# Performance work log

Hardware: AMD Instinct MI355X
Metric: run time of the kernel (lower is better)

Reference implementation:

```python
import jax, jax.numpy as jnp
import numpy as np

D_MODEL = 512
N_HEADS = 8
HEAD_SIZE = 64


def setup_inputs() -> dict:
    key = jax.random.key(0)
    ks = jax.random.split(key, 6)
    B, T = 4, 2048
    x_q = jax.random.normal(ks[0], (B, T, D_MODEL), dtype=jnp.float32)
    s = 1.0 / np.sqrt(D_MODEL)
    # per-head q/k/v projection weights, stacked: [H, head_size, d_model]
    Wq = jax.random.normal(ks[1], (N_HEADS, HEAD_SIZE, D_MODEL), dtype=jnp.float32) * s
    Wk = jax.random.normal(ks[2], (N_HEADS, HEAD_SIZE, D_MODEL), dtype=jnp.float32) * s
    Wv = jax.random.normal(ks[3], (N_HEADS, HEAD_SIZE, D_MODEL), dtype=jnp.float32) * s
    Wp = jax.random.normal(ks[4], (D_MODEL, D_MODEL), dtype=jnp.float32) * s
    bp = jax.random.normal(ks[5], (D_MODEL,), dtype=jnp.float32) * 0.01
    return {"x_q": x_q, "Wq": Wq, "Wk": Wk, "Wv": Wv, "Wp": Wp, "bp": bp}


def reference(x_q, Wq, Wk, Wv, Wp, bp):
    B, T, C = x_q.shape  # C == d_model
    # per-head projections: [B, H, T, K]
    q = jnp.einsum('btd,hkd->bhtk', x_q, Wq)
    k = jnp.einsum('btd,hkd->bhtk', x_q, Wk)
    v = jnp.einsum('btd,hkd->bhtk', x_q, Wv)
    # NOTE: original scales by C**-0.5 with C = d_model (not head_size)
    scores = jnp.einsum('bhtk,bhsk->bhts', q, k) * (C ** -0.5)
    causal = jnp.tril(jnp.ones((T, T), dtype=bool))
    scores = jnp.where(causal, scores, -jnp.inf)
    wei = jax.nn.softmax(scores, axis=-1)  # dropout is identity in eval
    out = jnp.einsum('bhts,bhsk->bhtk', wei, v)
    # concat heads: [B, T, H*K] == [B, T, d_model]
    out = out.transpose(0, 2, 1, 3).reshape(B, T, C)
    return out @ Wp.T + bp
```

## Files before the change

kernel.cpp:

```cpp
#include <hip/hip_runtime.h>
#include <hip/hip_bf16.h>

using bf16x8 = __attribute__((ext_vector_type(8))) __bf16;
using f32x4  = __attribute__((ext_vector_type(4))) float;
using f32x16 = __attribute__((ext_vector_type(16))) float;
using i32x4  = __attribute__((ext_vector_type(4))) int;

#define MFMA_16x16x32(a, b, c) __builtin_amdgcn_mfma_f32_16x16x32_bf16((a), (b), (c), 0, 0, 0)
#define MFMA32(a, b, c)        __builtin_amdgcn_mfma_f32_32x32x16_bf16((a), (b), (c), 0, 0, 0)

#define GLOAD16(g, l)                                                         \
    __builtin_amdgcn_global_load_lds(                                         \
        (const __attribute__((address_space(1))) unsigned int*)(g),           \
        (__attribute__((address_space(3))) unsigned int*)(l), 16, 0, 0)

__device__ __forceinline__ ushort f2bf(float f) {
    return __builtin_bit_cast(ushort, (__bf16)f);
}
__device__ __forceinline__ float bf2f(ushort u) {
    union { unsigned int i; float f; } x; x.i = ((unsigned int)u) << 16; return x.f;
}
__device__ __forceinline__ unsigned pk_bf16(float lo, float hi) {
    unsigned r;
    asm volatile("v_cvt_pk_bf16_f32 %0, %1, %2" : "=v"(r) : "v"(lo), "v"(hi));
    return r;
}
__device__ __forceinline__ void pl32_swap(unsigned &a, unsigned &b) {
    asm volatile("v_permlane32_swap_b32 %0, %1" : "+v"(a), "+v"(b));
}

#define ENC(t, a, b) ((t) | ((a) << 8) | ((b) << 16))
__device__ __constant__ unsigned UT[22] = {
    ENC(9,0,10), ENC(8,0,9),  ENC(15,0,8), ENC(15,8,16), ENC(14,0,8), ENC(7,0,8),
    ENC(14,8,15),ENC(13,0,7), ENC(13,7,14),ENC(12,0,7),  ENC(6,0,7),
    ENC(12,7,13),ENC(11,0,6), ENC(11,6,12),ENC(10,0,6),  ENC(5,0,6),
    ENC(10,6,11),ENC(4,0,5),  ENC(3,0,4),  ENC(2,0,3),   ENC(1,0,2),  ENC(0,0,1)
};

__global__ __launch_bounds__(256) void cvt_bf16(
    const float* __restrict__ in, ushort* __restrict__ out, int n)
{
    const int i = (blockIdx.x * 256 + threadIdx.x) * 8;
    if (i + 8 <= n) {
        const f32x4 a = *(const f32x4*)(in + i);
        const f32x4 b = *(const f32x4*)(in + i + 4);
        union { ushort u[8]; i32x4 w; } p;
        #pragma unroll
        for (int j = 0; j < 4; ++j) { p.u[j] = f2bf(a[j]); p.u[4 + j] = f2bf(b[j]); }
        *(i32x4*)(out + i) = p.w;
    }
}

__global__ __launch_bounds__(256) void cvt_fused(
    const float* __restrict__ x, ushort* __restrict__ xbf, int nx, int nxb,
    const float* __restrict__ w0, const float* __restrict__ w1,
    const float* __restrict__ w2, ushort* __restrict__ wbf,
    const float* __restrict__ wp, ushort* __restrict__ wpbf)
{
    const int b = (int)blockIdx.x;
    if (b < nxb) {
        const int i = (b * 256 + (int)threadIdx.x) * 8;
        if (i + 8 <= nx) {
            const f32x4 a = *(const f32x4*)(x + i);
            const f32x4 c = *(const f32x4*)(x + i + 4);
            union { ushort u[8]; i32x4 w; } p;
            #pragma unroll
            for (int j = 0; j < 4; ++j) { p.u[j] = f2bf(a[j]); p.u[4 + j] = f2bf(c[j]); }
            *(i32x4*)(xbf + i) = p.w;
        }
    } else if (b < nxb + 384) {
        const int i = ((b - nxb) * 256 + (int)threadIdx.x) * 8;
        const int w = i >> 18, off = i & 262143;
        const float* src = (w == 0) ? w0 : ((w == 1) ? w1 : w2);
        const f32x4 a = *(const f32x4*)(src + off);
        const f32x4 c = *(const f32x4*)(src + off + 4);
        union { ushort u[8]; i32x4 v; } p;
        #pragma unroll
        for (int j = 0; j < 4; ++j) { p.u[j] = f2bf(a[j]); p.u[4 + j] = f2bf(c[j]); }
        *(i32x4*)(wbf + i) = p.v;
    } else {
        const int i = ((b - nxb - 384) * 256 + (int)threadIdx.x) * 8;
        const f32x4 a = *(const f32x4*)(wp + i);
        const f32x4 c = *(const f32x4*)(wp + i + 4);
        union { ushort u[8]; i32x4 v; } p;
        #pragma unroll
        for (int j = 0; j < 4; ++j) { p.u[j] = f2bf(a[j]); p.u[4 + j] = f2bf(c[j]); }
        *(i32x4*)(wpbf + i) = p.v;
    }
}

__global__ __launch_bounds__(256) void gemm_qkv3(
    const ushort* __restrict__ A, const ushort* __restrict__ Wbf,
    float qscale, ushort* __restrict__ qb, ushort* __restrict__ kb,
    ushort* __restrict__ vb)
{
    __shared__ ushort lA[2][128][32];
    __shared__ ushort lB[2][128][32];
    const int wsel = blockIdx.y >> 2;
    const int n0 = (blockIdx.y & 3) * 128;
    const ushort* W = Wbf + wsel * 262144;
    ushort* out = (wsel == 0) ? qb : ((wsel == 1) ? kb : vb);
    const float scale = (wsel == 0) ? qscale : 1.0f;

    const int m0 = blockIdx.x * 128;
    const int tid  = threadIdx.x;
    const int lane = tid & 63;
    const int wave = tid >> 6;
    const int wr = (wave >> 1) * 64, wc = (wave & 1) * 64;
    const int frow = lane & 15;
    const int fkp  = (((lane >> 4) ^ ((lane >> 1) & 3))) * 8;

    const int srw  = lane >> 2;
    const int scol = ((lane & 3) ^ ((lane >> 3) & 3)) * 8;

    f32x4 acc[4][4] = {};
    auto stage = [&](int k0, int b) {
        #pragma unroll
        for (int i = 0; i < 2; ++i) {
            const int rb = (wave * 2 + i) * 16;
            GLOAD16(A + (size_t)(m0 + rb + srw) * 512 + k0 + scol, &lA[b][rb][0]);
            GLOAD16(W + (size_t)(n0 + rb + srw) * 512 + k0 + scol, &lB[b][rb][0]);
        }
    };

    stage(0, 0);
    for (int t = 0; t < 16; ++t) {
        const int p = t & 1;
        __syncthreads();
        if (t + 1 < 16) stage((t + 1) * 32, p ^ 1);

        bf16x8 af[4], bg[4];
        #pragma unroll
        for (int m = 0; m < 4; ++m) af[m] = *(const bf16x8*)&lA[p][wr + m * 16 + frow][fkp];
        #pragma unroll
        for (int n = 0; n < 4; ++n) bg[n] = *(const bf16x8*)&lB[p][wc + n * 16 + frow][fkp];
        #pragma unroll
        for (int m = 0; m < 4; ++m)
            #pragma unroll
            for (int n = 0; n < 4; ++n)
                acc[m][n] = MFMA_16x16x32(af[m], bg[n], acc[m][n]);
    }

    const int rbase = (lane >> 4) * 4;
    const int ccol  = lane & 15;
    if (wsel == 2) {
        #pragma unroll
        for (int m = 0; m < 4; ++m)
            #pragma unroll
            for (int n = 0; n < 4; ++n) {
                const int col = n0 + wc + n * 16 + ccol;
                const int row0 = m0 + wr + m * 16 + rbase;
                unsigned long long u = 0;
                #pragma unroll
                for (int r = 0; r < 4; ++r)
                    u |= ((unsigned long long)f2bf(acc[m][n][r])) << (16 * r);
                const size_t idx = ((size_t)((row0 >> 11) * 8 + (col >> 6)) * 64
                                    + (col & 63)) * 2048 + (row0 & 2047);
                *(unsigned long long*)(out + idx) = u;
            }
    } else {
        #pragma unroll
        for (int m = 0; m < 4; ++m)
            #pragma unroll
            for (int n = 0; n < 4; ++n) {
                const int col = n0 + wc + n * 16 + ccol;
                #pragma unroll
                for (int r = 0; r < 4; ++r) {
                    const int row = m0 + wr + m * 16 + rbase + r;
                    out[(((row >> 11) * 8 + (col >> 6)) * 2048 + (row & 2047)) * 64 + (col & 63)]
                        = f2bf(acc[m][n][r] * scale);
                }
            }
    }
}

__global__ __launch_bounds__(256) void gemm_out(
    const ushort* __restrict__ A, const ushort* __restrict__ W,
    const float* __restrict__ bias, float* __restrict__ out)
{
    __shared__ ushort lA[2][128][32];
    __shared__ ushort lB[2][128][32];
    const int m0 = blockIdx.x * 128;
    const int n0 = blockIdx.y * 128;
    const int tid  = threadIdx.x;
    const int lane = tid & 63;
    const int wave = tid >> 6;
    const int wr = (wave >> 1) * 64, wc = (wave & 1) * 64;
    const int frow = lane & 15;
    const int fkp  = (((lane >> 4) ^ ((lane >> 1) & 3))) * 8;

    const int srw  = lane >> 2;
    const int scol = ((lane & 3) ^ ((lane >> 3) & 3)) * 8;

    f32x4 acc[4][4] = {};
    auto stage = [&](int k0, int b) {
        #pragma unroll
        for (int i = 0; i < 2; ++i) {
            const int rb = (wave * 2 + i) * 16;
            const int row = m0 + rb + srw, c = k0 + scol;
            const size_t ia = (((size_t)(row >> 11) * 8 + (c >> 6)) * 2048
                               + (row & 2047)) * 64 + (c & 63);
            GLOAD16(A + ia, &lA[b][rb][0]);
            GLOAD16(W + (size_t)(n0 + rb + srw) * 512 + k0 + scol, &lB[b][rb][0]);
        }
    };

    stage(0, 0);
    for (int t = 0; t < 16; ++t) {
        const int p = t & 1;
        __syncthreads();
        if (t + 1 < 16) stage((t + 1) * 32, p ^ 1);

        bf16x8 af[4], bg[4];
        #pragma unroll
        for (int m = 0; m < 4; ++m) af[m] = *(const bf16x8*)&lA[p][wr + m * 16 + frow][fkp];
        #pragma unroll
        for (int n = 0; n < 4; ++n) bg[n] = *(const bf16x8*)&lB[p][wc + n * 16 + frow][fkp];
        #pragma unroll
        for (int m = 0; m < 4; ++m)
            #pragma unroll
            for (int n = 0; n < 4; ++n)
                acc[m][n] = MFMA_16x16x32(af[m], bg[n], acc[m][n]);
    }

    const int rbase = (lane >> 4) * 4;
    const int ccol  = lane & 15;
    #pragma unroll
    for (int m = 0; m < 4; ++m)
        #pragma unroll
        for (int n = 0; n < 4; ++n) {
            const int col = n0 + wc + n * 16 + ccol;
            const float bv = bias[col];
            #pragma unroll
            for (int r = 0; r < 4; ++r) {
                const int row = m0 + wr + m * 16 + rbase + r;
                out[row * 512 + col] = acc[m][n][r] + bv;
            }
        }
}

__global__ __launch_bounds__(256, 2) void attn_kernel(
    const ushort* __restrict__ q, const ushort* __restrict__ k,
    const ushort* __restrict__ vt, ushort* __restrict__ att,
    ushort* __restrict__ Ob, float* __restrict__ Mb, float* __restrict__ Lb)
{
    __shared__ ushort lK[2][2][64][64];
    __shared__ ushort lV[2][2][64][64];

    const int NH   = (int)gridDim.x / 22;
    const int n    = (int)blockIdx.x;
    const int unit = n / NH;
    const int bh   = n % NH;
    const unsigned ue = UT[unit];
    const int tile = (int)(ue & 0xff);
    const int c0   = (int)((ue >> 8) & 0xff);
    const int c1   = (int)((ue >> 16) & 0xff);
    const int qt0  = tile * 128;

    const ushort* Q  = q  + (size_t)bh * 2048 * 64;
    const ushort* K  = k  + (size_t)bh * 2048 * 64;
    const ushort* VT = vt + (size_t)bh * 2048 * 64;
    ushort* O = att + (size_t)bh * 2048 * 64;

    const int tid = threadIdx.x;
    const int wv  = tid >> 6;
    const int l   = tid & 63;
    const int ql  = l & 31;
    const int hi  = l >> 5;
    const int wrow0 = qt0 + wv * 32;
    const int qrow  = wrow0 + ql;
    const int wmax  = wrow0 + 31;
    const int qkey  = ql & 7;
    const float LOG2E = 1.44269504088896f;

    const int srow = tid >> 2;
    const int sg   = (tid & 3) * 2;
    const int skey = srow & 7;

    bf16x8 aq[4];
    #pragma unroll
    for (int kk = 0; kk < 4; ++kk)
        aq[kk] = *(const bf16x8*)(Q + (size_t)qrow * 64 + kk * 16 + hi * 8);

    f32x16 o0 = {}, o1 = {};
    float mrun = -30000.0f, lrun = 0.0f;

    i32x4 kr[2][2], vr[2][2];
    auto loadG = [&](int s0) {
        #pragma unroll
        for (int hf = 0; hf < 2; ++hf) {
            const ushort* kp = K + (size_t)(s0 + hf * 64 + srow) * 64 + (tid & 3) * 16;
            kr[hf][0] = *(const i32x4*)(kp);
            kr[hf][1] = *(const i32x4*)(kp + 8);
            const ushort* vp = VT + (size_t)srow * 2048 + s0 + hf * 64 + (tid & 3) * 16;
            vr[hf][0] = *(const i32x4*)(vp);
            vr[hf][1] = *(const i32x4*)(vp + 8);
        }
    };
    auto writeL = [&](int b) {
        #pragma unroll
        for (int hf = 0; hf < 2; ++hf) {
            *(i32x4*)&lK[b][hf][srow][((sg    ) ^ skey) * 8] = kr[hf][0];
            *(i32x4*)&lK[b][hf][srow][((sg + 1) ^ skey) * 8] = kr[hf][1];
            *(i32x4*)&lV[b][hf][srow][((sg    ) ^ skey) * 8] = vr[hf][0];
            *(i32x4*)&lV[b][hf][srow][((sg + 1) ^ skey) * 8] = vr[hf][1];
        }
    };

    loadG(c0 * 128);
    writeL(c0 & 1);
    if (c0 + 1 < c1) loadG((c0 + 1) * 128);

    for (int T = c0; T < c1; ++T) {
        const int p  = T & 1;
        const int s0 = T * 128;
        __syncthreads();
        if (T + 1 < c1) writeL(p ^ 1);
        if (T + 2 < c1) loadG(s0 + 256);

        const bool act1 = (s0 + 64 <= wmax);

        f32x16 sa0 = {}, sb0 = {}, sa1 = {}, sb1 = {};
        #pragma unroll
        for (int kk = 0; kk < 4; ++kk) {
            const bf16x8 a0 = *(const bf16x8*)&lK[p][0][ql]     [((2 * kk + hi) ^ qkey) * 8];
            const bf16x8 b0 = *(const bf16x8*)&lK[p][0][32 + ql][((2 * kk + hi) ^ qkey) * 8];
            sa0 = MFMA32(a0, aq[kk], sa0);
            sb0 = MFMA32(b0, aq[kk], sb0);
        }
        if (act1) {
            #pragma unroll
            for (int kk = 0; kk < 4; ++kk) {
                const bf16x8 a1 = *(const bf16x8*)&lK[p][1][ql]     [((2 * kk + hi) ^ qkey) * 8];
                const bf16x8 b1 = *(const bf16x8*)&lK[p][1][32 + ql][((2 * kk + hi) ^ qkey) * 8];
                sa1 = MFMA32(a1, aq[kk], sa1);
                sb1 = MFMA32(b1, aq[kk], sb1);
            }
        }

        if (s0 + 63 > wrow0) {
            #pragma unroll
            for (int rr = 0; rr < 16; ++rr) {
                const int cr = (rr & 3) + 8 * (rr >> 2) + 4 * hi;
                if (s0 + cr > qrow)      sa0[rr] = -30000.0f;
                if (s0 + 32 + cr > qrow) sb0[rr] = -30000.0f;
            }
        }
        if (act1 && (s0 + 127 > wrow0)) {
            #pragma unroll
            for (int rr = 0; rr < 16; ++rr) {
                const int cr = (rr & 3) + 8 * (rr >> 2) + 4 * hi;
                if (s0 + 64 + cr > qrow) sa1[rr] = -30000.0f;
                if (s0 + 96 + cr > qrow) sb1[rr] = -30000.0f;
            }
        }

        float tm[16];
        #pragma unroll
        for (int rr = 0; rr < 16; ++rr) tm[rr] = fmaxf(sa0[rr], sb0[rr]);
        if (act1) {
            #pragma unroll
            for (int rr = 0; rr < 16; ++rr)
                tm[rr] = fmaxf(tm[rr], fmaxf(sa1[rr], sb1[rr]));
        }
        #pragma unroll
        for (int s = 8; s > 0; s >>= 1)
            #pragma unroll
            for (int rr = 0; rr < s; ++rr) tm[rr] = fmaxf(tm[rr], tm[rr + s]);
        float pmax = fmaxf(tm[0], __shfl_xor(tm[0], 32));

        if (__any(pmax > mrun + 8.0f)) {
            const float mnew  = fmaxf(mrun, pmax);
            const float alpha = exp2f((mrun - mnew) * LOG2E);
            mrun = mnew;
            lrun *= alpha;
            #pragma unroll
            for (int rr = 0; rr < 16; ++rr) {
                const float ar = __shfl(alpha, (rr & 3) + 8 * (rr >> 2) + 4 * hi);
                o0[rr] *= ar; o1[rr] *= ar;
            }
        }

        const float mb = mrun * LOG2E;
        #pragma unroll
        for (int rr = 0; rr < 16; ++rr) {
            sa0[rr] = exp2f(fmaf(sa0[rr], LOG2E, -mb));
            sb0[rr] = exp2f(fmaf(sb0[rr], LOG2E, -mb));
        }
        if (act1) {
            #pragma unroll
            for (int rr = 0; rr < 16; ++rr) {
                sa1[rr] = exp2f(fmaf(sa1[rr], LOG2E, -mb));
                sb1[rr] = exp2f(fmaf(sb1[rr], LOG2E, -mb));
            }
        }

        float tu[16];
        #pragma unroll
        for (int rr = 0; rr < 16; ++rr) tu[rr] = sa0[rr] + sb0[rr];
        if (act1) {
            #pragma unroll
            for (int rr = 0; rr < 16; ++rr) tu[rr] += sa1[rr] + sb1[rr];
        }
        #pragma unroll
        for (int s = 8; s > 0; s >>= 1)
            #pragma unroll
            for (int rr = 0; rr < s; ++rr) tu[rr] += tu[rr + s];
        lrun += tu[0] + __shfl_xor(tu[0], 32);

        {
            unsigned paw[4][4];
            #pragma unroll
            for (int ks = 0; ks < 4; ++ks) {
                const int e = 2 * ks, f = 2 * ks + 1;
                const int ra = 4 * (e & 3), rb = 4 * (f & 3);
                unsigned A0, A1, B0, B1;
                if (e >> 2) { A0 = pk_bf16(sb0[ra], sb0[ra + 1]); A1 = pk_bf16(sb0[ra + 2], sb0[ra + 3]); }
                else        { A0 = pk_bf16(sa0[ra], sa0[ra + 1]); A1 = pk_bf16(sa0[ra + 2], sa0[ra + 3]); }
                if (f >> 2) { B0 = pk_bf16(sb0[rb], sb0[rb + 1]); B1 = pk_bf16(sb0[rb + 2], sb0[rb + 3]); }
                else        { B0 = pk_bf16(sa0[rb], sa0[rb + 1]); B1 = pk_bf16(sa0[rb + 2], sa0[rb + 3]); }
                pl32_swap(A0, B0);
                pl32_swap(A1, B1);
                paw[ks][0] = A0; paw[ks][1] = A1; paw[ks][2] = B0; paw[ks][3] = B1;
            }
            #pragma unroll
            for (int ks = 0; ks < 4; ++ks) {
                union { unsigned w[4]; bf16x8 v; } u;
                u.w[0] = paw[ks][0]; u.w[1] = paw[ks][1];
                u.w[2] = paw[ks][2]; u.w[3] = paw[ks][3];
                const bf16x8 v0 = *(const bf16x8*)&lV[p][0][ql]     [((2 * ks + hi) ^ qkey) * 8];
                const bf16x8 v1 = *(const bf16x8*)&lV[p][0][32 + ql][((2 * ks + hi) ^ qkey) * 8];
                o0 = MFMA32(u.v, v0, o0);
                o1 = MFMA32(u.v, v1, o1);
            }
        }
        if (act1) {
            unsigned paw[4][4];
            #pragma unroll
            for (int ks = 0; ks < 4; ++ks) {
                const int e = 2 * ks, f = 2 * ks + 1;
                const int ra = 4 * (e & 3), rb = 4 * (f & 3);
                unsigned A0, A1, B0, B1;
                if (e >> 2) { A0 = pk_bf16(sb1[ra], sb1[ra + 1]); A1 = pk_bf16(sb1[ra + 2], sb1[ra + 3]); }
                else        { A0 = pk_bf16(sa1[ra], sa1[ra + 1]); A1 = pk_bf16(sa1[ra + 2], sa1[ra + 3]); }
                if (f >> 2) { B0 = pk_bf16(sb1[rb], sb1[rb + 1]); B1 = pk_bf16(sb1[rb + 2], sb1[rb + 3]); }
                else        { B0 = pk_bf16(sa1[rb], sa1[rb + 1]); B1 = pk_bf16(sa1[rb + 2], sa1[rb + 3]); }
                pl32_swap(A0, B0);
                pl32_swap(A1, B1);
                paw[ks][0] = A0; paw[ks][1] = A1; paw[ks][2] = B0; paw[ks][3] = B1;
            }
            #pragma unroll
            for (int ks = 0; ks < 4; ++ks) {
                union { unsigned w[4]; bf16x8 v; } u;
                u.w[0] = paw[ks][0]; u.w[1] = paw[ks][1];
                u.w[2] = paw[ks][2]; u.w[3] = paw[ks][3];
                const bf16x8 v0 = *(const bf16x8*)&lV[p][1][ql]     [((2 * ks + hi) ^ qkey) * 8];
                const bf16x8 v1 = *(const bf16x8*)&lV[p][1][32 + ql][((2 * ks + hi) ^ qkey) * 8];
                o0 = MFMA32(u.v, v0, o0);
                o1 = MFMA32(u.v, v1, o1);
            }
        }
    }

    const float linv = 1.0f / fmaxf(lrun, 1e-30f);
    if (tile < 10) {
        #pragma unroll
        for (int rr = 0; rr < 16; ++rr) {
            const int cr = (rr & 3) + 8 * (rr >> 2) + 4 * hi;
            const float li = __shfl(linv, cr);
            const int row = wrow0 + cr;
            O[(size_t)row * 64 + ql]      = f2bf(o0[rr] * li);
            O[(size_t)row * 64 + 32 + ql] = f2bf(o1[rr] * li);
        }
    } else {
        const int pi    = bh * 6 + (tile - 10);
        const int chunk = (c0 != 0) ? 1 : 0;
        ushort* ob = Ob + (size_t)(pi * 2 + chunk) * 128 * 64 + wv * 32 * 64;
        #pragma unroll
        for (int rr = 0; rr < 16; ++rr) {
            const int cr = (rr & 3) + 8 * (rr >> 2) + 4 * hi;
            const float li = __shfl(linv, cr);
            ob[(size_t)cr * 64 + ql]      = f2bf(o0[rr] * li);
            ob[(size_t)cr * 64 + 32 + ql] = f2bf(o1[rr] * li);
        }
        if (hi == 0) {
            const int ri = (pi * 2 + chunk) * 128 + wv * 32 + ql;
            Mb[ri] = mrun;
            Lb[ri] = lrun;
        }
    }
}

__global__ __launch_bounds__(256) void merge_part(
    const ushort* __restrict__ Ob, const float* __restrict__ Mb,
    const float* __restrict__ Lb, ushort* __restrict__ att)
{
    const int pi   = (int)blockIdx.x;
    const int bh   = pi / 6;
    const int tile = 10 + pi % 6;
    const int t    = threadIdx.x;
    const int row  = t >> 1;
    const int ch   = (t & 1) * 32;
    const float LOG2E = 1.44269504088896f;

    const int riA = (pi * 2 + 0) * 128 + row;
    const int riB = (pi * 2 + 1) * 128 + row;
    const float mA = Mb[riA], lA = Lb[riA];
    const float mB = Mb[riB], lB = Lb[riB];
    const float M  = fmaxf(mA, mB);
    const float wA = lA * exp2f((mA - M) * LOG2E);
    const float wB = lB * exp2f((mB - M) * LOG2E);
    const float inv = 1.0f / fmaxf(wA + wB, 1e-30f);

    const ushort* oa = Ob + (size_t)(pi * 2 + 0) * 128 * 64 + (size_t)row * 64 + ch;
    const ushort* obp = Ob + (size_t)(pi * 2 + 1) * 128 * 64 + (size_t)row * 64 + ch;
    ushort* dst = att + (size_t)bh * 2048 * 64 + (size_t)(tile * 128 + row) * 64 + ch;
    #pragma unroll
    for (int j = 0; j < 32; ++j)
        dst[j] = f2bf((wA * bf2f(oa[j]) + wB * bf2f(obp[j])) * inv);
}

extern "C" void kernel_launch(void* const* d_in, const int* in_sizes, int n_in,
                              void* d_out, int out_size, void* d_ws, size_t ws_size,
                              hipStream_t stream) {
    const float* x  = (const float*)d_in[0];
    const float* Wq = (const float*)d_in[1];
    const float* Wk = (const float*)d_in[2];
    const float* Wv = (const float*)d_in[3];
    const float* Wp = (const float*)d_in[4];
    const float* bp = (const float*)d_in[5];
    float* out = (float*)d_out;

    const size_t NEL  = 4u * 8u * 2048u * 64u;
    const size_t NELB = 8u * 2048u * 64u;
    const size_t WPN  = 262144u;
    const float qscale = 0.04419417382415922f;

    if (ws_size >= 3u * NEL * sizeof(ushort)) {
        ushort* xbf = (ushort*)d_out;
        ushort* qb  = xbf + NEL;
        ushort* kb  = (ushort*)d_ws;
        ushort* vb  = kb + NEL;
        ushort* ab  = vb + NEL;
        ushort* wbf = ab;
        const int nxb = (int)(NEL / (256 * 8));

        ushort* Ob = xbf;
        float*  Mb = (float*)(xbf + 192u * 2u * 128u * 64u);
        float*  Lb = Mb + 192u * 2u * 128u;

        const bool fuse_wp = ws_size >= (3u * NEL + WPN) * sizeof(ushort);
        ushort* wpbf = fuse_wp ? (ab + NEL) : kb;
        if (fuse_wp) {
            hipLaunchKernelGGL(cvt_fused, dim3(nxb + 384 + 128), dim3(256), 0, stream,
                               x, xbf, (int)NEL, nxb, Wq, Wk, Wv, wbf, Wp, wpbf);
        } else {
            hipLaunchKernelGGL(cvt_fused, dim3(nxb + 384), dim3(256), 0, stream,
                               x, xbf, (int)NEL, nxb, Wq, Wk, Wv, wbf, Wp, wpbf);
        }
        hipLaunchKernelGGL(gemm_qkv3, dim3(64, 12), dim3(256), 0, stream,
                           xbf, wbf, qscale, qb, kb, vb);
        hipLaunchKernelGGL(attn_kernel, dim3(22 * 32), dim3(256), 0, stream,
                           qb, kb, vb, ab, Ob, Mb, Lb);
        hipLaunchKernelGGL(merge_part, dim3(6 * 32), dim3(256), 0, stream, Ob, Mb, Lb, ab);
        if (!fuse_wp)
            hipLaunchKernelGGL(cvt_bf16, dim3(128), dim3(256), 0, stream, Wp, wpbf, (int)WPN);
        hipLaunchKernelGGL(gemm_out, dim3(64, 4), dim3(256), 0, stream, ab, wpbf, bp, out);
    } else {
        ushort* kb  = (ushort*)d_ws;
        ushort* vb  = kb + NELB;
        ushort* ab  = vb + NELB;
        ushort* wbf = ab;
        for (int b = 0; b < 4; ++b) {
            const float* xb = x + (size_t)b * 2048u * 512u;
            float* ob = out + (size_t)b * 2048u * 512u;
            ushort* xbf  = (ushort*)ob;
            ushort* qb   = xbf + NELB;
            ushort* wpbf = kb;
            ushort* Ob = xbf;
            float*  Mb = (float*)(xbf + 48u * 2u * 128u * 64u);
            float*  Lb = Mb + 48u * 2u * 128u;
            hipLaunchKernelGGL(cvt_fused, dim3((int)(NELB / (256 * 8)) + 384), dim3(256), 0, stream,
                               xb, xbf, (int)NELB, (int)(NELB / (256 * 8)), Wq, Wk, Wv, wbf,
                               Wp, wpbf);
            hipLaunchKernelGGL(gemm_qkv3, dim3(16, 12), dim3(256), 0, stream,
                               xbf, wbf, qscale, qb, kb, vb);
            hipLaunchKernelGGL(attn_kernel, dim3(22 * 8), dim3(256), 0, stream,
                               qb, kb, vb, ab, Ob, Mb, Lb);
            hipLaunchKernelGGL(merge_part, dim3(6 * 8), dim3(256), 0, stream, Ob, Mb, Lb, ab);
            hipLaunchKernelGGL(cvt_bf16, dim3(128), dim3(256), 0, stream, Wp, wpbf, (int)WPN);
            hipLaunchKernelGGL(gemm_out, dim3(16, 4), dim3(256), 0, stream, ab, wpbf, bp, ob);
        }
    }
}
```

Baseline: 92.07 us.

## Single-buffer K/V LDS tiles and raise attention occupancy to four blocks

Replaces the double-buffered LDS staging of K and V with a single buffer, halving shared memory per block to 32 KB, and raises launch bounds from 2 to 4 blocks per CU. Each iteration now writes the register-prefetched tile to LDS between two barriers, then issues the next global prefetch. This trades intra-block overlap for more resident waves to hide latency, at the cost of an extra barrier per tile and a tighter register budget that may cause spills.

```diff
diff --git a/kernel.cpp b/kernel.cpp
--- a/kernel.cpp
+++ b/kernel.cpp
@@ -239,13 +239,13 @@
         }
 }
 
-__global__ __launch_bounds__(256, 2) void attn_kernel(
+__global__ __launch_bounds__(256, 4) void attn_kernel(
     const ushort* __restrict__ q, const ushort* __restrict__ k,
     const ushort* __restrict__ vt, ushort* __restrict__ att,
     ushort* __restrict__ Ob, float* __restrict__ Mb, float* __restrict__ Lb)
 {
-    __shared__ ushort lK[2][2][64][64];
-    __shared__ ushort lV[2][2][64][64];
+    __shared__ ushort lK[2][64][64];
+    __shared__ ushort lV[2][64][64];
 
     const int NH   = (int)gridDim.x / 22;
     const int n    = (int)blockIdx.x;
@@ -297,42 +297,40 @@
             vr[hf][1] = *(const i32x4*)(vp + 8);
         }
     };
-    auto writeL = [&](int b) {
+    auto writeL = [&]() {
         #pragma unroll
         for (int hf = 0; hf < 2; ++hf) {
-            *(i32x4*)&lK[b][hf][srow][((sg    ) ^ skey) * 8] = kr[hf][0];
-            *(i32x4*)&lK[b][hf][srow][((sg + 1) ^ skey) * 8] = kr[hf][1];
-            *(i32x4*)&lV[b][hf][srow][((sg    ) ^ skey) * 8] = vr[hf][0];
-            *(i32x4*)&lV[b][hf][srow][((sg + 1) ^ skey) * 8] = vr[hf][1];
+            *(i32x4*)&lK[hf][srow][((sg    ) ^ skey) * 8] = kr[hf][0];
+            *(i32x4*)&lK[hf][srow][((sg + 1) ^ skey) * 8] = kr[hf][1];
+            *(i32x4*)&lV[hf][srow][((sg    ) ^ skey) * 8] = vr[hf][0];
+            *(i32x4*)&lV[hf][srow][((sg + 1) ^ skey) * 8] = vr[hf][1];
         }
     };
 
     loadG(c0 * 128);
-    writeL(c0 & 1);
-    if (c0 + 1 < c1) loadG((c0 + 1) * 128);
 
     for (int T = c0; T < c1; ++T) {
-        const int p  = T & 1;
         const int s0 = T * 128;
         __syncthreads();
-        if (T + 1 < c1) writeL(p ^ 1);
-        if (T + 2 < c1) loadG(s0 + 256);
+        writeL();
+        __syncthreads();
+        if (T + 1 < c1) loadG(s0 + 128);
 
         const bool act1 = (s0 + 64 <= wmax);
 
         f32x16 sa0 = {}, sb0 = {}, sa1 = {}, sb1 = {};
         #pragma unroll
         for (int kk = 0; kk < 4; ++kk) {
-            const bf16x8 a0 = *(const bf16x8*)&lK[p][0][ql]     [((2 * kk + hi) ^ qkey) * 8];
-            const bf16x8 b0 = *(const bf16x8*)&lK[p][0][32 + ql][((2 * kk + hi) ^ qkey) * 8];
+            const bf16x8 a0 = *(const bf16x8*)&lK[0][ql]     [((2 * kk + hi) ^ qkey) * 8];
+            const bf16x8 b0 = *(const bf16x8*)&lK[0][32 + ql][((2 * kk + hi) ^ qkey) * 8];
             sa0 = MFMA32(a0, aq[kk], sa0);
             sb0 = MFMA32(b0, aq[kk], sb0);
         }
         if (act1) {
             #pragma unroll
             for (int kk = 0; kk < 4; ++kk) {
-                const bf16x8 a1 = *(const bf16x8*)&lK[p][1][ql]     [((2 * kk + hi) ^ qkey) * 8];
-                const bf16x8 b1 = *(const bf16x8*)&lK[p][1][32 + ql][((2 * kk + hi) ^ qkey) * 8];
+                const bf16x8 a1 = *(const bf16x8*)&lK[1][ql]     [((2 * kk + hi) ^ qkey) * 8];
+                const bf16x8 b1 = *(const bf16x8*)&lK[1][32 + ql][((2 * kk + hi) ^ qkey) * 8];
                 sa1 = MFMA32(a1, aq[kk], sa1);
                 sb1 = MFMA32(b1, aq[kk], sb1);
             }
@@ -428,8 +426,8 @@
                 union { unsigned w[4]; bf16x8 v; } u;
                 u.w[0] = paw[ks][0]; u.w[1] = paw[ks][1];
                 u.w[2] = paw[ks][2]; u.w[3] = paw[ks][3];
-                const bf16x8 v0 = *(const bf16x8*)&lV[p][0][ql]     [((2 * ks + hi) ^ qkey) * 8];
-                const bf16x8 v1 = *(const bf16x8*)&lV[p][0][32 + ql][((2 * ks + hi) ^ qkey) * 8];
+                const bf16x8 v0 = *(const bf16x8*)&lV[0][ql]     [((2 * ks + hi) ^ qkey) * 8];
+                const bf16x8 v1 = *(const bf16x8*)&lV[0][32 + ql][((2 * ks + hi) ^ qkey) * 8];
                 o0 = MFMA32(u.v, v0, o0);
                 o1 = MFMA32(u.v, v1, o1);
             }
@@ -454,8 +452,8 @@
                 union { unsigned w[4]; bf16x8 v; } u;
                 u.w[0] = paw[ks][0]; u.w[1] = paw[ks][1];
                 u.w[2] = paw[ks][2]; u.w[3] = paw[ks][3];
-                const bf16x8 v0 = *(const bf16x8*)&lV[p][1][ql]     [((2 * ks + hi) ^ qkey) * 8];
-                const bf16x8 v1 = *(const bf16x8*)&lV[p][1][32 + ql][((2 * ks + hi) ^ qkey) * 8];
+                const bf16x8 v0 = *(const bf16x8*)&lV[1][ql]     [((2 * ks + hi) ^ qkey) * 8];
+                const bf16x8 v1 = *(const bf16x8*)&lV[1][32 + ql][((2 * ks + hi) ^ qkey) * 8];
                 o0 = MFMA32(u.v, v0, o0);
                 o1 = MFMA32(u.v, v1, o1);
             }
```

Result: slower. 214.4 us (+132.9%).
